# Optimization experiments

Hardware: AMD Instinct MI355X
Metric: run time of the kernel (lower is better)

Reference implementation:

```python
import jax, jax.numpy as jnp
import numpy as np

B, T, I = 16384, 50, 5
H = 128
PRED_LEN = 12


def _uniform(key, shape, bound):
    return jax.random.uniform(key, shape, jnp.float32, -bound, bound)


def setup_inputs() -> dict:
    key = jax.random.key(0)
    ks = jax.random.split(key, 12)
    bound = 1.0 / np.sqrt(H)  # PyTorch LSTM/Linear default init
    return {
        "x": jax.random.normal(ks[0], (B, T, I), jnp.float32),
        "enc_Wih": _uniform(ks[1], (4 * H, I), bound),
        "enc_Whh": _uniform(ks[2], (4 * H, H), bound),
        "enc_bih": _uniform(ks[3], (4 * H,), bound),
        "enc_bhh": _uniform(ks[4], (4 * H,), bound),
        "dec_Wih": _uniform(ks[5], (4 * H, I), bound),
        "dec_Whh": _uniform(ks[6], (4 * H, H), bound),
        "dec_bih": _uniform(ks[7], (4 * H,), bound),
        "dec_bhh": _uniform(ks[8], (4 * H,), bound),
        "lin_W": _uniform(ks[9], (2, H), bound),
        "lin_b": _uniform(ks[10], (2,), bound),
    }


def _lstm_cell(x_t, h, c, Wih, Whh, bih, bhh):
    # PyTorch gate order: i, f, g, o
    gates = x_t @ Wih.T + h @ Whh.T + (bih + bhh)  # [B, 4H]
    i, f, g, o = jnp.split(gates, 4, axis=-1)
    i = jax.nn.sigmoid(i)
    f = jax.nn.sigmoid(f)
    g = jnp.tanh(g)
    o = jax.nn.sigmoid(o)
    c_new = f * c + i * g
    h_new = o * jnp.tanh(c_new)
    return h_new, c_new


def reference(x, enc_Wih, enc_Whh, enc_bih, enc_bhh,
              dec_Wih, dec_Whh, dec_bih, dec_bhh, lin_W, lin_b):
    b = x.shape[0]
    h0 = jnp.zeros((b, H), x.dtype)
    c0 = jnp.zeros((b, H), x.dtype)

    # ---- encoder LSTM over the history sequence ----
    def enc_step(carry, x_t):
        h, c = carry
        h, c = _lstm_cell(x_t, h, c, enc_Wih, enc_Whh, enc_bih, enc_bhh)
        return (h, c), None

    (h, c), _ = jax.lax.scan(enc_step, (h0, c0), jnp.swapaxes(x, 0, 1))

    static_context = x[:, -1, 2:]          # [B, I-2]
    last_velocity = x[:, -1, :2]           # [B, 2]
    dec_in0 = jnp.concatenate([last_velocity, static_context], axis=1)  # [B, I]

    def dec_step(carry, _):
        h, c, dec_in = carry
        h, c = _lstm_cell(dec_in, h, c, dec_Wih, dec_Whh, dec_bih, dec_bhh)
        pred = h @ lin_W.T + lin_b                      # [B, 2]
        dec_in = jnp.concatenate([pred, static_context], axis=1)
        return (h, c, dec_in), pred

    _, preds = jax.lax.scan(dec_step, (h, c, dec_in0), None, length=PRED_LEN)
    return jnp.swapaxes(preds, 0, 1)  # [B, pred_len, 2]
```

## Files before the change

kernel.cpp:

```cpp
#include <hip/hip_runtime.h>
#include <cstdint>

#define TT 50
#define II 5
#define PRED 12

typedef _Float16 f16;
typedef _Float16 f16x8 __attribute__((ext_vector_type(8)));
typedef float f32x4 __attribute__((ext_vector_type(4)));

__global__ void prep_weights(const float* __restrict__ Wih, const float* __restrict__ Whh,
                             const float* __restrict__ bih, const float* __restrict__ bhh,
                             f16* __restrict__ outw) {
    int f = blockIdx.x * 256 + threadIdx.x;
    if (f >= 81920) return;
    int j  = f & 7;
    int c  = (f >> 3) & 15;
    int q  = (f >> 7) & 3;
    int t2 = f >> 9;
    int kc = t2 % 5;
    int wg = t2 / 5;
    int w = wg >> 2, gsub = wg & 3;
    int g = gsub * 128 + w * 16 + c;
    int k = kc * 32 + q * 8 + j;
    float v;
    if (k < 128)       v = Whh[g * 128 + k];
    else if (k < 133)  v = Wih[g * 5 + (k - 128)];
    else if (k == 133) v = bih[g] + bhh[g];
    else               v = 0.f;
    outw[f] = (f16)v;
}

__device__ __forceinline__ float fsig(float x) {
    return __builtin_amdgcn_rcpf(1.f + __builtin_amdgcn_exp2f(-1.4426950408889634f * x));
}
__device__ __forceinline__ float ftanh(float x) {
    return 1.f - 2.f * __builtin_amdgcn_rcpf(1.f + __builtin_amdgcn_exp2f(2.885390081777927f * x));
}

__global__ __launch_bounds__(512, 2)
void lstm_kernel(const float* __restrict__ x,
                 const f16* __restrict__ wfrag,
                 const float* __restrict__ linW, const float* __restrict__ linB,
                 float* __restrict__ out) {
    __shared__ __align__(16) unsigned char state[64 * 512];
    __shared__ float predpart[8][64][2];

    const int tid  = threadIdx.x;
    const int lane = tid & 63;
    const int w    = tid >> 6;
    const int q    = lane >> 4;
    const int cl   = lane & 15;
    const int s0   = blockIdx.x * 64;
    const int jb   = w * 16 + q * 4;
    const int physh = ((jb >> 3) ^ (2 * cl)) & 31;
    const int hoff  = (jb & 7) * 2;

    f16x8 wr[4][5];
    {
        const f16x8* wp = (const f16x8*)wfrag;
        #pragma unroll
        for (int gs = 0; gs < 4; ++gs) {
            #pragma unroll
            for (int kc = 0; kc < 5; ++kc)
                wr[gs][kc] = wp[((w * 4 + gs) * 5 + kc) * 64 + lane];
        }
    }
    float w0r[4], w1r[4];
    #pragma unroll
    for (int idx = 0; idx < 4; ++idx) {
        w0r[idx] = linW[jb + idx];
        w1r[idx] = linW[128 + jb + idx];
    }
    float sc0 = 0.f, sc1 = 0.f, sc2 = 0.f;
    if (tid < 64) {
        const float* xr = x + (size_t)(s0 + tid) * (TT * II) + 49 * II;
        sc0 = xr[2]; sc1 = xr[3]; sc2 = xr[4];
    }
    {
        uint32_t* sp = (uint32_t*)state;
        #pragma unroll
        for (int r = 0; r < 16; ++r) sp[tid + r * 512] = 0u;
    }
    float creg[4][4];
    #pragma unroll
    for (int a = 0; a < 4; ++a)
        #pragma unroll
        for (int b = 0; b < 4; ++b) creg[a][b] = 0.f;

    __syncthreads();
    if (tid < 64) {
        const float* xr = x + (size_t)(s0 + tid) * (TT * II);
        union { f16 h[8]; uint4 u; } pk;
        pk.h[0] = (f16)xr[0]; pk.h[1] = (f16)xr[1]; pk.h[2] = (f16)xr[2];
        pk.h[3] = (f16)xr[3]; pk.h[4] = (f16)xr[4];
        pk.h[5] = (f16)1.f; pk.h[6] = (f16)0.f; pk.h[7] = (f16)0.f;
        int phys = 16 ^ (2 * (tid & 15));
        *(uint4*)(state + tid * 512 + phys * 16) = pk.u;
    }
    __syncthreads();

    f32x4 zero4 = {0.f, 0.f, 0.f, 0.f};

    #pragma unroll 1
    for (int t = 0; t < TT; ++t) {
        float xv0 = 0, xv1 = 0, xv2 = 0, xv3 = 0, xv4 = 0;
        if (tid < 64) {
            int tn = (t < TT - 1) ? t + 1 : TT - 1;
            const float* xr = x + (size_t)(s0 + tid) * (TT * II) + tn * II;
            xv0 = xr[0]; xv1 = xr[1]; xv2 = xr[2]; xv3 = xr[3]; xv4 = xr[4];
        }
        f32x4 acc[4][4];
        #pragma unroll
        for (int gs = 0; gs < 4; ++gs)
            #pragma unroll
            for (int ns = 0; ns < 4; ++ns) acc[gs][ns] = zero4;

        #pragma unroll
        for (int ns = 0; ns < 4; ++ns) {
            const int srow = ns * 16 + cl;
            #pragma unroll
            for (int kc = 0; kc < 5; ++kc) {
                const int phys = (kc * 4 + q) ^ (2 * cl);
                f16x8 bf = *(const f16x8*)(state + srow * 512 + phys * 16);
                acc[0][ns] = __builtin_amdgcn_mfma_f32_16x16x32_f16(wr[0][kc], bf, acc[0][ns], 0, 0, 0);
                acc[1][ns] = __builtin_amdgcn_mfma_f32_16x16x32_f16(wr[1][kc], bf, acc[1][ns], 0, 0, 0);
                acc[2][ns] = __builtin_amdgcn_mfma_f32_16x16x32_f16(wr[2][kc], bf, acc[2][ns], 0, 0, 0);
                acc[3][ns] = __builtin_amdgcn_mfma_f32_16x16x32_f16(wr[3][kc], bf, acc[3][ns], 0, 0, 0);
            }
        }
        uint2 hp[4];
        #pragma unroll
        for (int ns = 0; ns < 4; ++ns) {
            union { f16 h[4]; uint2 u; } pk;
            #pragma unroll
            for (int idx = 0; idx < 4; ++idx) {
                float ii = fsig(acc[0][ns][idx]);
                float ff = fsig(acc[1][ns][idx]);
                float gg = ftanh(acc[2][ns][idx]);
                float oo = fsig(acc[3][ns][idx]);
                float cn = ff * creg[ns][idx] + ii * gg;
                creg[ns][idx] = cn;
                pk.h[idx] = (f16)(oo * ftanh(cn));
            }
            hp[ns] = pk.u;
        }
        __syncthreads();
        #pragma unroll
        for (int ns = 0; ns < 4; ++ns)
            *(uint2*)(state + (ns * 16 + cl) * 512 + physh * 16 + hoff) = hp[ns];
        if (tid < 64) {
            union { f16 h[8]; uint4 u; } pk;
            pk.h[0] = (f16)xv0; pk.h[1] = (f16)xv1; pk.h[2] = (f16)xv2;
            pk.h[3] = (f16)xv3; pk.h[4] = (f16)xv4;
            pk.h[5] = (f16)1.f; pk.h[6] = (f16)0.f; pk.h[7] = (f16)0.f;
            int phys = 16 ^ (2 * (tid & 15));
            *(uint4*)(state + tid * 512 + phys * 16) = pk.u;
        }
        __syncthreads();
    }

    {
        const f16x8* wp = (const f16x8*)(wfrag + 81920);
        #pragma unroll
        for (int gs = 0; gs < 4; ++gs) {
            #pragma unroll
            for (int kc = 0; kc < 5; ++kc)
                wr[gs][kc] = wp[((w * 4 + gs) * 5 + kc) * 64 + lane];
        }
    }

    #pragma unroll 1
    for (int td = 0; td < PRED; ++td) {
        f32x4 acc[4][4];
        #pragma unroll
        for (int gs = 0; gs < 4; ++gs)
            #pragma unroll
            for (int ns = 0; ns < 4; ++ns) acc[gs][ns] = zero4;

        #pragma unroll
        for (int ns = 0; ns < 4; ++ns) {
            const int srow = ns * 16 + cl;
            #pragma unroll
            for (int kc = 0; kc < 5; ++kc) {
                const int phys = (kc * 4 + q) ^ (2 * cl);
                f16x8 bf = *(const f16x8*)(state + srow * 512 + phys * 16);
                acc[0][ns] = __builtin_amdgcn_mfma_f32_16x16x32_f16(wr[0][kc], bf, acc[0][ns], 0, 0, 0);
                acc[1][ns] = __builtin_amdgcn_mfma_f32_16x16x32_f16(wr[1][kc], bf, acc[1][ns], 0, 0, 0);
                acc[2][ns] = __builtin_amdgcn_mfma_f32_16x16x32_f16(wr[2][kc], bf, acc[2][ns], 0, 0, 0);
                acc[3][ns] = __builtin_amdgcn_mfma_f32_16x16x32_f16(wr[3][kc], bf, acc[3][ns], 0, 0, 0);
            }
        }
        uint2 hp[4];
        float p0[4], p1[4];
        #pragma unroll
        for (int ns = 0; ns < 4; ++ns) {
            union { f16 h[4]; uint2 u; } pk;
            p0[ns] = 0.f; p1[ns] = 0.f;
            #pragma unroll
            for (int idx = 0; idx < 4; ++idx) {
                float ii = fsig(acc[0][ns][idx]);
                float ff = fsig(acc[1][ns][idx]);
                float gg = ftanh(acc[2][ns][idx]);
                float oo = fsig(acc[3][ns][idx]);
                float cn = ff * creg[ns][idx] + ii * gg;
                creg[ns][idx] = cn;
                float hv = oo * ftanh(cn);
                p0[ns] += hv * w0r[idx];
                p1[ns] += hv * w1r[idx];
                pk.h[idx] = (f16)hv;
            }
            hp[ns] = pk.u;
        }
        #pragma unroll
        for (int ns = 0; ns < 4; ++ns) {
            p0[ns] += __shfl_xor(p0[ns], 16);
            p0[ns] += __shfl_xor(p0[ns], 32);
            p1[ns] += __shfl_xor(p1[ns], 16);
            p1[ns] += __shfl_xor(p1[ns], 32);
        }
        if (q == 0) {
            #pragma unroll
            for (int ns = 0; ns < 4; ++ns) {
                predpart[w][ns * 16 + cl][0] = p0[ns];
                predpart[w][ns * 16 + cl][1] = p1[ns];
            }
        }
        __syncthreads();
        #pragma unroll
        for (int ns = 0; ns < 4; ++ns)
            *(uint2*)(state + (ns * 16 + cl) * 512 + physh * 16 + hoff) = hp[ns];
        if (tid < 64) {
            float a0 = linB[0], a1 = linB[1];
            #pragma unroll
            for (int ww = 0; ww < 8; ++ww) {
                a0 += predpart[ww][tid][0];
                a1 += predpart[ww][tid][1];
            }
            float2 o2; o2.x = a0; o2.y = a1;
            *(float2*)(out + (size_t)(s0 + tid) * (PRED * 2) + td * 2) = o2;
            union { f16 h[8]; uint4 u; } pk;
            pk.h[0] = (f16)a0; pk.h[1] = (f16)a1;
            pk.h[2] = (f16)sc0; pk.h[3] = (f16)sc1; pk.h[4] = (f16)sc2;
            pk.h[5] = (f16)1.f; pk.h[6] = (f16)0.f; pk.h[7] = (f16)0.f;
            int phys = 16 ^ (2 * (tid & 15));
            *(uint4*)(state + tid * 512 + phys * 16) = pk.u;
        }
        __syncthreads();
    }
}

extern "C" void kernel_launch(void* const* d_in, const int* in_sizes, int n_in,
                              void* d_out, int out_size, void* d_ws, size_t ws_size,
                              hipStream_t stream) {
    (void)in_sizes; (void)n_in; (void)out_size; (void)ws_size;
    const float* x    = (const float*)d_in[0];
    const float* eWih = (const float*)d_in[1];
    const float* eWhh = (const float*)d_in[2];
    const float* ebih = (const float*)d_in[3];
    const float* ebhh = (const float*)d_in[4];
    const float* dWih = (const float*)d_in[5];
    const float* dWhh = (const float*)d_in[6];
    const float* dbih = (const float*)d_in[7];
    const float* dbhh = (const float*)d_in[8];
    const float* linW = (const float*)d_in[9];
    const float* linB = (const float*)d_in[10];
    f16* wfrag = (f16*)d_ws;

    prep_weights<<<320, 256, 0, stream>>>(eWih, eWhh, ebih, ebhh, wfrag);
    prep_weights<<<320, 256, 0, stream>>>(dWih, dWhh, dbih, dbhh, wfrag + 81920);
    lstm_kernel<<<256, 512, 0, stream>>>(x, wfrag, linW, linB, (float*)d_out);
}
```

Baseline: 281.0 us.

## Halve samples per block, double-buffer state, fuse gate math, merge weight prep

Each block now handles 32 samples instead of 64, with launch bounds raised to 4 blocks per CU and twice as many blocks, which trades MFMA work per block for more resident waves to hide the recurrent latency. The LSTM state buffer in shared memory is double-buffered so h is written straight into the next buffer, removing one barrier per step. Gate nonlinearities are rewritten to share reciprocals, cutting the number of rcp calls per element, and tanh(c) clamps its input. The two weight-prep launches are merged into one, and the decoder-only loads are moved after the encoder loop. The extra blocks each reload the full weight fragments into registers.

```diff
diff --git a/kernel.cpp b/kernel.cpp
--- a/kernel.cpp
+++ b/kernel.cpp
@@ -4,20 +4,30 @@
 #define TT 50
 #define II 5
 #define PRED 12
+#define SAMP 32
+#define NS 2
 
 typedef _Float16 f16;
 typedef _Float16 f16x8 __attribute__((ext_vector_type(8)));
 typedef float f32x4 __attribute__((ext_vector_type(4)));
 
-__global__ void prep_weights(const float* __restrict__ Wih, const float* __restrict__ Whh,
-                             const float* __restrict__ bih, const float* __restrict__ bhh,
+__global__ void prep_weights(const float* __restrict__ eWih, const float* __restrict__ eWhh,
+                             const float* __restrict__ ebih, const float* __restrict__ ebhh,
+                             const float* __restrict__ dWih, const float* __restrict__ dWhh,
+                             const float* __restrict__ dbih, const float* __restrict__ dbhh,
                              f16* __restrict__ outw) {
     int f = blockIdx.x * 256 + threadIdx.x;
-    if (f >= 81920) return;
-    int j  = f & 7;
-    int c  = (f >> 3) & 15;
-    int q  = (f >> 7) & 3;
-    int t2 = f >> 9;
+    if (f >= 2 * 81920) return;
+    int ph = (f >= 81920);
+    int fl = f - ph * 81920;
+    const float* Wih = ph ? dWih : eWih;
+    const float* Whh = ph ? dWhh : eWhh;
+    const float* bih = ph ? dbih : ebih;
+    const float* bhh = ph ? dbhh : ebhh;
+    int j  = fl & 7;
+    int c  = (fl >> 3) & 15;
+    int q  = (fl >> 7) & 3;
+    int t2 = fl >> 9;
     int kc = t2 % 5;
     int wg = t2 / 5;
     int w = wg >> 2, gsub = wg & 3;
@@ -31,27 +41,23 @@
     outw[f] = (f16)v;
 }
 
-__device__ __forceinline__ float fsig(float x) {
-    return __builtin_amdgcn_rcpf(1.f + __builtin_amdgcn_exp2f(-1.4426950408889634f * x));
-}
-__device__ __forceinline__ float ftanh(float x) {
-    return 1.f - 2.f * __builtin_amdgcn_rcpf(1.f + __builtin_amdgcn_exp2f(2.885390081777927f * x));
-}
-
-__global__ __launch_bounds__(512, 2)
+#define K1 1.4426950408889634f
+#define K2 2.8853900817779268f
+
+__global__ __launch_bounds__(512, 4)
 void lstm_kernel(const float* __restrict__ x,
                  const f16* __restrict__ wfrag,
                  const float* __restrict__ linW, const float* __restrict__ linB,
                  float* __restrict__ out) {
-    __shared__ __align__(16) unsigned char state[64 * 512];
-    __shared__ float predpart[8][64][2];
+    __shared__ __align__(16) unsigned char state[2][SAMP * 512];
+    __shared__ float predpart[8][SAMP][2];
 
     const int tid  = threadIdx.x;
     const int lane = tid & 63;
     const int w    = tid >> 6;
     const int q    = lane >> 4;
     const int cl   = lane & 15;
-    const int s0   = blockIdx.x * 64;
+    const int s0   = blockIdx.x * SAMP;
     const int jb   = w * 16 + q * 4;
     const int physh = ((jb >> 3) ^ (2 * cl)) & 31;
     const int hoff  = (jb & 7) * 2;
@@ -66,37 +72,26 @@
                 wr[gs][kc] = wp[((w * 4 + gs) * 5 + kc) * 64 + lane];
         }
     }
-    float w0r[4], w1r[4];
-    #pragma unroll
-    for (int idx = 0; idx < 4; ++idx) {
-        w0r[idx] = linW[jb + idx];
-        w1r[idx] = linW[128 + jb + idx];
-    }
-    float sc0 = 0.f, sc1 = 0.f, sc2 = 0.f;
-    if (tid < 64) {
-        const float* xr = x + (size_t)(s0 + tid) * (TT * II) + 49 * II;
-        sc0 = xr[2]; sc1 = xr[3]; sc2 = xr[4];
-    }
     {
         uint32_t* sp = (uint32_t*)state;
         #pragma unroll
         for (int r = 0; r < 16; ++r) sp[tid + r * 512] = 0u;
     }
-    float creg[4][4];
+    float creg[NS][4];
     #pragma unroll
-    for (int a = 0; a < 4; ++a)
+    for (int a = 0; a < NS; ++a)
         #pragma unroll
         for (int b = 0; b < 4; ++b) creg[a][b] = 0.f;
 
     __syncthreads();
-    if (tid < 64) {
+    if (tid < SAMP) {
         const float* xr = x + (size_t)(s0 + tid) * (TT * II);
         union { f16 h[8]; uint4 u; } pk;
         pk.h[0] = (f16)xr[0]; pk.h[1] = (f16)xr[1]; pk.h[2] = (f16)xr[2];
         pk.h[3] = (f16)xr[3]; pk.h[4] = (f16)xr[4];
         pk.h[5] = (f16)1.f; pk.h[6] = (f16)0.f; pk.h[7] = (f16)0.f;
         int phys = 16 ^ (2 * (tid & 15));
-        *(uint4*)(state + tid * 512 + phys * 16) = pk.u;
+        *(uint4*)(&state[0][0] + tid * 512 + phys * 16) = pk.u;
     }
     __syncthreads();
 
@@ -104,58 +99,61 @@
 
     #pragma unroll 1
     for (int t = 0; t < TT; ++t) {
+        unsigned char* cur = &state[t & 1][0];
+        unsigned char* nxt = &state[(t + 1) & 1][0];
         float xv0 = 0, xv1 = 0, xv2 = 0, xv3 = 0, xv4 = 0;
-        if (tid < 64) {
+        if (tid < SAMP) {
             int tn = (t < TT - 1) ? t + 1 : TT - 1;
             const float* xr = x + (size_t)(s0 + tid) * (TT * II) + tn * II;
             xv0 = xr[0]; xv1 = xr[1]; xv2 = xr[2]; xv3 = xr[3]; xv4 = xr[4];
         }
-        f32x4 acc[4][4];
+        f32x4 acc[4][NS];
         #pragma unroll
         for (int gs = 0; gs < 4; ++gs)
             #pragma unroll
-            for (int ns = 0; ns < 4; ++ns) acc[gs][ns] = zero4;
-
-        #pragma unroll
-        for (int ns = 0; ns < 4; ++ns) {
+            for (int ns = 0; ns < NS; ++ns) acc[gs][ns] = zero4;
+
+        #pragma unroll
+        for (int ns = 0; ns < NS; ++ns) {
             const int srow = ns * 16 + cl;
             #pragma unroll
             for (int kc = 0; kc < 5; ++kc) {
                 const int phys = (kc * 4 + q) ^ (2 * cl);
-                f16x8 bf = *(const f16x8*)(state + srow * 512 + phys * 16);
+                f16x8 bf = *(const f16x8*)(cur + srow * 512 + phys * 16);
                 acc[0][ns] = __builtin_amdgcn_mfma_f32_16x16x32_f16(wr[0][kc], bf, acc[0][ns], 0, 0, 0);
                 acc[1][ns] = __builtin_amdgcn_mfma_f32_16x16x32_f16(wr[1][kc], bf, acc[1][ns], 0, 0, 0);
                 acc[2][ns] = __builtin_amdgcn_mfma_f32_16x16x32_f16(wr[2][kc], bf, acc[2][ns], 0, 0, 0);
                 acc[3][ns] = __builtin_amdgcn_mfma_f32_16x16x32_f16(wr[3][kc], bf, acc[3][ns], 0, 0, 0);
             }
         }
-        uint2 hp[4];
-        #pragma unroll
-        for (int ns = 0; ns < 4; ++ns) {
+        #pragma unroll
+        for (int ns = 0; ns < NS; ++ns) {
             union { f16 h[4]; uint2 u; } pk;
             #pragma unroll
             for (int idx = 0; idx < 4; ++idx) {
-                float ii = fsig(acc[0][ns][idx]);
-                float ff = fsig(acc[1][ns][idx]);
-                float gg = ftanh(acc[2][ns][idx]);
-                float oo = fsig(acc[3][ns][idx]);
-                float cn = ff * creg[ns][idx] + ii * gg;
+                float ea = __builtin_amdgcn_exp2f(acc[0][ns][idx] * -K1);
+                float ef = __builtin_amdgcn_exp2f(acc[1][ns][idx] * -K1);
+                float eg = __builtin_amdgcn_exp2f(acc[2][ns][idx] *  K2);
+                float eo = __builtin_amdgcn_exp2f(acc[3][ns][idx] * -K1);
+                float a1 = 1.f + ea, a2 = 1.f + ef, a3 = eg + 1.f, a4 = eg - 1.f;
+                float t1 = a1 * a3;
+                float N1 = fmaf(creg[ns][idx], t1, a4 * a2);
+                float cn = N1 * __builtin_amdgcn_rcpf(t1 * a2);
                 creg[ns][idx] = cn;
-                pk.h[idx] = (f16)(oo * ftanh(cn));
-            }
-            hp[ns] = pk.u;
-        }
-        __syncthreads();
-        #pragma unroll
-        for (int ns = 0; ns < 4; ++ns)
-            *(uint2*)(state + (ns * 16 + cl) * 512 + physh * 16 + hoff) = hp[ns];
-        if (tid < 64) {
+                float cc = fminf(fmaxf(cn, -15.f), 15.f);
+                float ec = __builtin_amdgcn_exp2f(cc * K2);
+                float hv = (ec - 1.f) * __builtin_amdgcn_rcpf((1.f + eo) * (ec + 1.f));
+                pk.h[idx] = (f16)hv;
+            }
+            *(uint2*)(nxt + (ns * 16 + cl) * 512 + physh * 16 + hoff) = pk.u;
+        }
+        if (tid < SAMP) {
             union { f16 h[8]; uint4 u; } pk;
             pk.h[0] = (f16)xv0; pk.h[1] = (f16)xv1; pk.h[2] = (f16)xv2;
             pk.h[3] = (f16)xv3; pk.h[4] = (f16)xv4;
             pk.h[5] = (f16)1.f; pk.h[6] = (f16)0.f; pk.h[7] = (f16)0.f;
             int phys = 16 ^ (2 * (tid & 15));
-            *(uint4*)(state + tid * 512 + phys * 16) = pk.u;
+            *(uint4*)(nxt + tid * 512 + phys * 16) = pk.u;
         }
         __syncthreads();
     }
@@ -169,51 +167,69 @@
                 wr[gs][kc] = wp[((w * 4 + gs) * 5 + kc) * 64 + lane];
         }
     }
+    float w0r[4], w1r[4];
+    #pragma unroll
+    for (int idx = 0; idx < 4; ++idx) {
+        w0r[idx] = linW[jb + idx];
+        w1r[idx] = linW[128 + jb + idx];
+    }
+    float sc0 = 0.f, sc1 = 0.f, sc2 = 0.f, lb0 = 0.f, lb1 = 0.f;
+    if (tid < SAMP) {
+        const float* xr = x + (size_t)(s0 + tid) * (TT * II) + 49 * II;
+        sc0 = xr[2]; sc1 = xr[3]; sc2 = xr[4];
+        lb0 = linB[0]; lb1 = linB[1];
+    }
 
     #pragma unroll 1
     for (int td = 0; td < PRED; ++td) {
-        f32x4 acc[4][4];
+        unsigned char* cur = &state[td & 1][0];
+        unsigned char* nxt = &state[(td + 1) & 1][0];
+        f32x4 acc[4][NS];
         #pragma unroll
         for (int gs = 0; gs < 4; ++gs)
             #pragma unroll
-            for (int ns = 0; ns < 4; ++ns) acc[gs][ns] = zero4;
-
-        #pragma unroll
-        for (int ns = 0; ns < 4; ++ns) {
+            for (int ns = 0; ns < NS; ++ns) acc[gs][ns] = zero4;
+
+        #pragma unroll
+        for (int ns = 0; ns < NS; ++ns) {
             const int srow = ns * 16 + cl;
             #pragma unroll
             for (int kc = 0; kc < 5; ++kc) {
                 const int phys = (kc * 4 + q) ^ (2 * cl);
-                f16x8 bf = *(const f16x8*)(state + srow * 512 + phys * 16);
+                f16x8 bf = *(const f16x8*)(cur + srow * 512 + phys * 16);
                 acc[0][ns] = __builtin_amdgcn_mfma_f32_16x16x32_f16(wr[0][kc], bf, acc[0][ns], 0, 0, 0);
                 acc[1][ns] = __builtin_amdgcn_mfma_f32_16x16x32_f16(wr[1][kc], bf, acc[1][ns], 0, 0, 0);
                 acc[2][ns] = __builtin_amdgcn_mfma_f32_16x16x32_f16(wr[2][kc], bf, acc[2][ns], 0, 0, 0);
                 acc[3][ns] = __builtin_amdgcn_mfma_f32_16x16x32_f16(wr[3][kc], bf, acc[3][ns], 0, 0, 0);
             }
         }
-        uint2 hp[4];
-        float p0[4], p1[4];
-        #pragma unroll
-        for (int ns = 0; ns < 4; ++ns) {
+        float p0[NS], p1[NS];
+        #pragma unroll
+        for (int ns = 0; ns < NS; ++ns) {
             union { f16 h[4]; uint2 u; } pk;
             p0[ns] = 0.f; p1[ns] = 0.f;
             #pragma unroll
             for (int idx = 0; idx < 4; ++idx) {
-                float ii = fsig(acc[0][ns][idx]);
-                float ff = fsig(acc[1][ns][idx]);
-                float gg = ftanh(acc[2][ns][idx]);
-                float oo = fsig(acc[3][ns][idx]);
-                float cn = ff * creg[ns][idx] + ii * gg;
+                float ea = __builtin_amdgcn_exp2f(acc[0][ns][idx] * -K1);
+                float ef = __builtin_amdgcn_exp2f(acc[1][ns][idx] * -K1);
+                float eg = __builtin_amdgcn_exp2f(acc[2][ns][idx] *  K2);
+                float eo = __builtin_amdgcn_exp2f(acc[3][ns][idx] * -K1);
+                float a1 = 1.f + ea, a2 = 1.f + ef, a3 = eg + 1.f, a4 = eg - 1.f;
+                float t1 = a1 * a3;
+                float N1 = fmaf(creg[ns][idx], t1, a4 * a2);
+                float cn = N1 * __builtin_amdgcn_rcpf(t1 * a2);
                 creg[ns][idx] = cn;
-                float hv = oo * ftanh(cn);
-                p0[ns] += hv * w0r[idx];
-                p1[ns] += hv * w1r[idx];
+                float cc = fminf(fmaxf(cn, -15.f), 15.f);
+                float ec = __builtin_amdgcn_exp2f(cc * K2);
+                float hv = (ec - 1.f) * __builtin_amdgcn_rcpf((1.f + eo) * (ec + 1.f));
+                p0[ns] = fmaf(hv, w0r[idx], p0[ns]);
+                p1[ns] = fmaf(hv, w1r[idx], p1[ns]);
                 pk.h[idx] = (f16)hv;
             }
-            hp[ns] = pk.u;
-        }
-        #pragma unroll
-        for (int ns = 0; ns < 4; ++ns) {
+            *(uint2*)(nxt + (ns * 16 + cl) * 512 + physh * 16 + hoff) = pk.u;
+        }
+        #pragma unroll
+        for (int ns = 0; ns < NS; ++ns) {
             p0[ns] += __shfl_xor(p0[ns], 16);
             p0[ns] += __shfl_xor(p0[ns], 32);
             p1[ns] += __shfl_xor(p1[ns], 16);
@@ -221,17 +237,14 @@
         }
         if (q == 0) {
             #pragma unroll
-            for (int ns = 0; ns < 4; ++ns) {
+            for (int ns = 0; ns < NS; ++ns) {
                 predpart[w][ns * 16 + cl][0] = p0[ns];
                 predpart[w][ns * 16 + cl][1] = p1[ns];
             }
         }
         __syncthreads();
-        #pragma unroll
-        for (int ns = 0; ns < 4; ++ns)
-            *(uint2*)(state + (ns * 16 + cl) * 512 + physh * 16 + hoff) = hp[ns];
-        if (tid < 64) {
-            float a0 = linB[0], a1 = linB[1];
+        if (tid < SAMP) {
+            float a0 = lb0, a1 = lb1;
             #pragma unroll
             for (int ww = 0; ww < 8; ++ww) {
                 a0 += predpart[ww][tid][0];
@@ -244,7 +257,7 @@
             pk.h[2] = (f16)sc0; pk.h[3] = (f16)sc1; pk.h[4] = (f16)sc2;
             pk.h[5] = (f16)1.f; pk.h[6] = (f16)0.f; pk.h[7] = (f16)0.f;
             int phys = 16 ^ (2 * (tid & 15));
-            *(uint4*)(state + tid * 512 + phys * 16) = pk.u;
+            *(uint4*)(nxt + tid * 512 + phys * 16) = pk.u;
         }
         __syncthreads();
     }
@@ -267,7 +280,7 @@
     const float* linB = (const float*)d_in[10];
     f16* wfrag = (f16*)d_ws;
 
-    prep_weights<<<320, 256, 0, stream>>>(eWih, eWhh, ebih, ebhh, wfrag);
-    prep_weights<<<320, 256, 0, stream>>>(dWih, dWhh, dbih, dbhh, wfrag + 81920);
-    lstm_kernel<<<256, 512, 0, stream>>>(x, wfrag, linW, linB, (float*)d_out);
+    prep_weights<<<640, 256, 0, stream>>>(eWih, eWhh, ebih, ebhh,
+                                          dWih, dWhh, dbih, dbhh, wfrag);
+    lstm_kernel<<<512, 512, 0, stream>>>(x, wfrag, linW, linB, (float*)d_out);
 }
```

Result: slower. 932.9 us (+232.0%).
